# Optimization experiments

Measured on AMD Instinct MI355X. Metric: run time of the kernel, lower is better.

## Reference

```python
import jax, jax.numpy as jnp
import numpy as np

INPUT_DIM = 4096
BATCH = 64
E_PER = 262144  # edges per graph
MIN_SP = 0.3


def setup_inputs() -> dict:
    key = jax.random.key(0)
    k1, k2, k3 = jax.random.split(key, 3)
    E = BATCH * E_PER
    edge_index = jax.random.randint(k1, (2, E), 0, INPUT_DIM, dtype=jnp.int64)
    edge_attr = jax.random.normal(k2, (E,), dtype=jnp.float32)
    ptr = jnp.arange(BATCH + 1, dtype=jnp.int64)
    # learned parameter (xavier-normal-ish init)
    std = float(np.sqrt(2.0 / (INPUT_DIM + INPUT_DIM)))
    weight_mask = jax.random.normal(k3, (INPUT_DIM, INPUT_DIM), dtype=jnp.float32) * std
    return {"edge_index": edge_index, "edge_attr": edge_attr, "ptr": ptr, "weight_mask": weight_mask}


def reference(edge_index, edge_attr, ptr, weight_mask):
    B = ptr.shape[0] - 1
    E = edge_index.shape[1]
    e_per = E // B
    # symmetric sigmoid mask (dropout is None -> identity)
    sym = jax.nn.sigmoid(weight_mask.T + weight_mask)
    # x_reshape: [B, e_per]
    x = edge_attr.reshape(B, e_per)
    # edge_ind_reshape: [B, 2, e_per]
    ei = edge_index.T.reshape(B, e_per, 2).transpose(0, 2, 1)
    # gather mask weights for batch-0 edges
    src = ei[0, 0]
    dst = ei[0, 1]
    w = sym[src, dst]  # [e_per]
    num_rm = int(e_per * MIN_SP)  # static count of pruned edges
    order = jnp.argsort(w)
    pruned = order[:num_rm]
    kept = jnp.sort(order[num_rm:])  # boolean-mask compaction preserves order
    mask = jnp.ones((e_per,), dtype=bool).at[pruned].set(False)
    # filtered edge_index: [B, 2, K] -> permute(1,0,2) -> [2, B*K]
    fei = jnp.take(ei, kept, axis=2)
    out_edge_index = fei.transpose(1, 0, 2).reshape(2, -1)
    # filtered edge_attr: [B, K] -> [B*K]
    out_edge_attr = jnp.take(x, kept, axis=1).reshape(-1)
    return out_edge_index, out_edge_attr, mask
```

## Files before the change

kernel.cpp:

```cpp
#include <hip/hip_runtime.h>
#include <stdint.h>
#include <math.h>

#define CAND_CAP 8192
typedef unsigned long long ull;
typedef long long ll;
typedef unsigned int uint;
typedef float __attribute__((ext_vector_type(4))) f4;
typedef int __attribute__((ext_vector_type(4))) i4;

struct Ctrl {
  int sel0;
  int r0;
  int binsel;
  int r_in;
  int ncand;
  int pad;
  ull Tpack;
};

__device__ __forceinline__ uint fkey(float f) {
  uint u = __float_as_uint(f);
  return (u & 0x80000000u) ? ~u : (u | 0x80000000u);
}

__global__ void __launch_bounds__(256) k_keys(
    const int* __restrict__ ei, const float* __restrict__ wm,
    ll E, int D, uint* __restrict__ key32, uint* __restrict__ hist0) {
  __shared__ uint sh[256];
  int t = threadIdx.x;
  sh[t] = 0u;
  __syncthreads();
  int v = blockIdx.x * 256 + t;
  int4 s4 = ((const int4*)ei)[v];
  int4 d4 = ((const int4*)(ei + E))[v];
  float a0 = wm[(ll)s4.x * D + d4.x], b0 = wm[(ll)d4.x * D + s4.x];
  float a1 = wm[(ll)s4.y * D + d4.y], b1 = wm[(ll)d4.y * D + s4.y];
  float a2 = wm[(ll)s4.z * D + d4.z], b2 = wm[(ll)d4.z * D + s4.z];
  float a3 = wm[(ll)s4.w * D + d4.w], b3 = wm[(ll)d4.w * D + s4.w];
  uint4 k;
  k.x = fkey((float)((double)a0 + (double)b0));
  k.y = fkey((float)((double)a1 + (double)b1));
  k.z = fkey((float)((double)a2 + (double)b2));
  k.w = fkey((float)((double)a3 + (double)b3));
  ((uint4*)key32)[v] = k;
  atomicAdd(&sh[k.x >> 24], 1u);
  atomicAdd(&sh[k.y >> 24], 1u);
  atomicAdd(&sh[k.z >> 24], 1u);
  atomicAdd(&sh[k.w >> 24], 1u);
  __syncthreads();
  if (sh[t]) atomicAdd(&hist0[t], sh[t]);
}

__global__ void k_pick0(const uint* __restrict__ hist0, int r, Ctrl* ctrl) {
  __shared__ uint sh[256];
  int t = threadIdx.x;
  uint c = hist0[t];
  sh[t] = c;
  __syncthreads();
  for (int off = 1; off < 256; off <<= 1) {
    uint v = sh[t];
    uint a = (t >= off) ? sh[t - off] : 0u;
    __syncthreads();
    sh[t] = v + a;
    __syncthreads();
  }
  uint incl = sh[t], excl = incl - c;
  if ((uint)r >= excl && (uint)r < incl) {
    ctrl->sel0 = t;
    ctrl->r0 = (int)((uint)r - excl);
  }
}

__global__ void __launch_bounds__(256) k_hist1(
    const uint* __restrict__ key32, const Ctrl* __restrict__ ctrl,
    uint* __restrict__ hist1) {
  __shared__ uint sh[256];
  int t = threadIdx.x;
  sh[t] = 0u;
  __syncthreads();
  uint sel0 = (uint)ctrl->sel0;
  uint4 k = ((const uint4*)key32)[blockIdx.x * 256 + t];
  if ((k.x >> 24) == sel0) atomicAdd(&sh[(k.x >> 16) & 0xFFu], 1u);
  if ((k.y >> 24) == sel0) atomicAdd(&sh[(k.y >> 16) & 0xFFu], 1u);
  if ((k.z >> 24) == sel0) atomicAdd(&sh[(k.z >> 16) & 0xFFu], 1u);
  if ((k.w >> 24) == sel0) atomicAdd(&sh[(k.w >> 16) & 0xFFu], 1u);
  __syncthreads();
  if (sh[t]) atomicAdd(&hist1[t], sh[t]);
}

__global__ void k_pick1(const uint* __restrict__ hist1, Ctrl* ctrl) {
  __shared__ uint sh[256];
  int t = threadIdx.x;
  uint c = hist1[t];
  sh[t] = c;
  __syncthreads();
  for (int off = 1; off < 256; off <<= 1) {
    uint v = sh[t];
    uint a = (t >= off) ? sh[t - off] : 0u;
    __syncthreads();
    sh[t] = v + a;
    __syncthreads();
  }
  uint incl = sh[t], excl = incl - c;
  uint r = (uint)ctrl->r0;
  if (r >= excl && r < incl) {
    ctrl->binsel = (ctrl->sel0 << 8) | t;
    ctrl->r_in = (int)(r - excl);
  }
}

__global__ void k_cand(const uint* __restrict__ key32, int N, Ctrl* ctrl,
                       ull* __restrict__ cand) {
  int e = blockIdx.x * blockDim.x + threadIdx.x;
  if (e >= N) return;
  uint k = key32[e];
  if ((int)(k >> 16) == ctrl->binsel) {
    int p = atomicAdd(&ctrl->ncand, 1);
    if (p < CAND_CAP) cand[p] = ((ull)k << 32) | (uint)e;
  }
}

__global__ void k_pickT(const ull* __restrict__ cand, Ctrl* ctrl) {
  int nc = ctrl->ncand;
  if (nc > CAND_CAP) nc = CAND_CAP;
  int r = ctrl->r_in;
  for (int o = threadIdx.x; o < nc; o += blockDim.x) {
    ull my = cand[o];
    int cnt = 0;
    for (int i = 0; i < nc; ++i) cnt += (cand[i] < my) ? 1 : 0;
    if (cnt == r) ctrl->Tpack = my;
  }
}

__device__ __forceinline__ int keptf(uint k, int e, ull T) {
  return ((((ull)k << 32) | (uint)e) > T) ? 1 : 0;
}

__global__ void __launch_bounds__(256) k_scanA(
    const uint* __restrict__ key32, const Ctrl* __restrict__ ctrl,
    int* __restrict__ pw, int* __restrict__ bs, float* __restrict__ mask_out) {
  __shared__ int sh[256];
  int t = threadIdx.x, blk = blockIdx.x;
  ull T = ctrl->Tpack;
  uint4 k4 = ((const uint4*)key32)[blk * 256 + t];
  int e0 = blk * 1024 + t * 4;
  int f0 = keptf(k4.x, e0, T), f1 = keptf(k4.y, e0 + 1, T);
  int f2 = keptf(k4.z, e0 + 2, T), f3 = keptf(k4.w, e0 + 3, T);
  int c = f0 + f1 + f2 + f3;
  sh[t] = c;
  __syncthreads();
  for (int off = 1; off < 256; off <<= 1) {
    int v = sh[t];
    int a = (t >= off) ? sh[t - off] : 0;
    __syncthreads();
    sh[t] = v + a;
    __syncthreads();
  }
  int excl = sh[t] - c;
  pw[blk * 256 + t] = (excl << 4) | f0 | (f1 << 1) | (f2 << 2) | (f3 << 3);
  ((float4*)mask_out)[blk * 256 + t] =
      make_float4((float)f0, (float)f1, (float)f2, (float)f3);
  if (t == 255) bs[blk] = sh[255];
}

__global__ void k_scanB(int* bs, int nb) {
  __shared__ int sh[256];
  int t = threadIdx.x;
  int v = (t < nb) ? bs[t] : 0;
  sh[t] = v;
  __syncthreads();
  for (int off = 1; off < 256; off <<= 1) {
    int x = sh[t];
    int a = (t >= off) ? sh[t - off] : 0;
    __syncthreads();
    sh[t] = x + a;
    __syncthreads();
  }
  if (t < nb) bs[t] = sh[t] - v;
}

__global__ void __launch_bounds__(256) k_compact(
    const int* __restrict__ pw, const int* __restrict__ bs,
    const int* __restrict__ ei, const float* __restrict__ attr,
    ll E, int N, int Kkeep, ll BK, float* __restrict__ out) {
  __shared__ float lds[4][3][264];
  int t = threadIdx.x;
  int w = t >> 6;
  int l = t & 63;
  int blk = blockIdx.x, b = blockIdx.y;
  int q = blk * 256 + t;
  int wv = pw[q];
  int flags = wv & 15;
  int excl = wv >> 4;
  int subbase = __shfl(excl, 0);
  int wlast = __shfl(wv, 63);
  int cnt = (wlast >> 4) + __popc(wlast & 15) - subbase;
  ll cb = (ll)b * N;
  i4 d0 = __builtin_nontemporal_load((const i4*)(ei + cb) + q);
  i4 d1 = __builtin_nontemporal_load((const i4*)(ei + E + cb) + q);
  f4 d2 = __builtin_nontemporal_load((const f4*)(attr + cb) + q);
  ll ob = (ll)b * Kkeep + bs[blk] + subbase;
  int al = (int)(ob & 3);
  int p = (excl - subbase) + al;
  float* L0 = lds[w][0];
  float* L1 = lds[w][1];
  float* L2 = lds[w][2];
  if (flags & 1) { L0[p] = (float)d0.x; L1[p] = (float)d1.x; L2[p] = d2.x; p++; }
  if (flags & 2) { L0[p] = (float)d0.y; L1[p] = (float)d1.y; L2[p] = d2.y; p++; }
  if (flags & 4) { L0[p] = (float)d0.z; L1[p] = (float)d1.z; L2[p] = d2.z; p++; }
  if (flags & 8) { L0[p] = (float)d0.w; L1[p] = (float)d1.w; L2[p] = d2.w; }
  __threadfence_block();
  int lo = al, hi = al + cnt;
  int nslot = (hi + 3) >> 2;
  ll gbase = ob - al;
  #pragma unroll
  for (int r = 0; r < 3; ++r) {
    const float* src = lds[w][r];
    float* dst = out + (ll)r * BK + gbase;
    for (int i = l; i < nslot; i += 64) {
      int j0 = 4 * i;
      f4 v = *(const f4*)(src + j0);
      if (j0 >= lo && j0 + 3 < hi) {
        __builtin_nontemporal_store(v, (f4*)(dst + j0));
      } else {
        if (j0 >= lo && j0 < hi)         __builtin_nontemporal_store(v.x, dst + j0);
        if (j0 + 1 >= lo && j0 + 1 < hi) __builtin_nontemporal_store(v.y, dst + j0 + 1);
        if (j0 + 2 >= lo && j0 + 2 < hi) __builtin_nontemporal_store(v.z, dst + j0 + 2);
        if (j0 + 3 >= lo && j0 + 3 < hi) __builtin_nontemporal_store(v.w, dst + j0 + 3);
      }
    }
  }
}

extern "C" void kernel_launch(void* const* d_in, const int* in_sizes, int n_in,
                              void* d_out, int out_size, void* d_ws, size_t ws_size,
                              hipStream_t stream) {
  const int* ei = (const int*)d_in[0];
  const float* attr = (const float*)d_in[1];
  const float* wm = (const float*)d_in[3];

  int B = in_sizes[2] - 1;
  ll E = (ll)in_sizes[0] / 2;
  int e_per = (int)(E / B);
  int D = (int)llround(sqrt((double)in_sizes[3]));
  int num_rm = (int)((double)e_per * 0.3);
  int Kkeep = e_per - num_rm;
  ll BK = (ll)B * Kkeep;
  int nb = (e_per + 1023) / 1024;

  char* w = (char*)d_ws;
  size_t off = 0;
  uint* key32 = (uint*)(w + off);  off += (size_t)e_per * 4;
  uint* hist0 = (uint*)(w + off);  off += 256 * 4;
  uint* hist1 = (uint*)(w + off);  off += 256 * 4;
  Ctrl* ctrl = (Ctrl*)(w + off);   off += 64;
  ull* cand = (ull*)(w + off);     off += (size_t)CAND_CAP * 8;
  int* bs = (int*)(w + off);       off += 1024;
  int* pw = (int*)(w + off);       off += (size_t)(e_per / 4) * 4;
  (void)ws_size; (void)n_in; (void)out_size;

  float* out = (float*)d_out;
  float* mask_out = out + 3 * BK;

  hipMemsetAsync(hist0, 0, 256 * 4 + 256 * 4 + 64, stream);
  k_keys<<<dim3(e_per / 1024), dim3(256), 0, stream>>>(ei, wm, E, D, key32, hist0);
  k_pick0<<<dim3(1), dim3(256), 0, stream>>>(hist0, num_rm - 1, ctrl);
  k_hist1<<<dim3(e_per / 1024), dim3(256), 0, stream>>>(key32, ctrl, hist1);
  k_pick1<<<dim3(1), dim3(256), 0, stream>>>(hist1, ctrl);
  k_cand<<<dim3(nb), dim3(1024), 0, stream>>>(key32, e_per, ctrl, cand);
  k_pickT<<<dim3(1), dim3(1024), 0, stream>>>(cand, ctrl);
  k_scanA<<<dim3(nb), dim3(256), 0, stream>>>(key32, ctrl, pw, bs, mask_out);
  k_scanB<<<dim3(1), dim3(256), 0, stream>>>(bs, nb);
  k_compact<<<dim3(nb, B), dim3(256), 0, stream>>>(pw, bs, ei, attr,
                                                   E, e_per, Kkeep, BK, out);
}
```

Before: 117.7 us.

## Process several graphs per compact block with software-prefetched inputs

k_compact now loops over 8 batch graphs per block instead of one. The per-position flags, prefix offsets and block base are loaded once and reused across those graphs, and the next graph's edge and attribute vectors are prefetched while the current one is written out. Input loads switch from nontemporal to regular loads. The grid gets smaller and each thread holds more registers, and the per-wave LDS staging buffer is reused across iterations with no explicit fence.

```diff
diff --git a/kernel.cpp b/kernel.cpp
--- a/kernel.cpp
+++ b/kernel.cpp
@@ -183,12 +183,13 @@
 __global__ void __launch_bounds__(256) k_compact(
     const int* __restrict__ pw, const int* __restrict__ bs,
     const int* __restrict__ ei, const float* __restrict__ attr,
-    ll E, int N, int Kkeep, ll BK, float* __restrict__ out) {
+    ll E, int N, int Kkeep, ll BK, int BPG, float* __restrict__ out) {
   __shared__ float lds[4][3][264];
   int t = threadIdx.x;
   int w = t >> 6;
   int l = t & 63;
-  int blk = blockIdx.x, b = blockIdx.y;
+  int blk = blockIdx.x;
+  int b0 = blockIdx.y * BPG;
   int q = blk * 256 + t;
   int wv = pw[q];
   int flags = wv & 15;
@@ -196,40 +197,54 @@
   int subbase = __shfl(excl, 0);
   int wlast = __shfl(wv, 63);
   int cnt = (wlast >> 4) + __popc(wlast & 15) - subbase;
-  ll cb = (ll)b * N;
-  i4 d0 = __builtin_nontemporal_load((const i4*)(ei + cb) + q);
-  i4 d1 = __builtin_nontemporal_load((const i4*)(ei + E + cb) + q);
-  f4 d2 = __builtin_nontemporal_load((const f4*)(attr + cb) + q);
-  ll ob = (ll)b * Kkeep + bs[blk] + subbase;
-  int al = (int)(ob & 3);
-  int p = (excl - subbase) + al;
+  int poff = excl - subbase;
+  ll obase = (ll)bs[blk] + subbase;
   float* L0 = lds[w][0];
   float* L1 = lds[w][1];
   float* L2 = lds[w][2];
-  if (flags & 1) { L0[p] = (float)d0.x; L1[p] = (float)d1.x; L2[p] = d2.x; p++; }
-  if (flags & 2) { L0[p] = (float)d0.y; L1[p] = (float)d1.y; L2[p] = d2.y; p++; }
-  if (flags & 4) { L0[p] = (float)d0.z; L1[p] = (float)d1.z; L2[p] = d2.z; p++; }
-  if (flags & 8) { L0[p] = (float)d0.w; L1[p] = (float)d1.w; L2[p] = d2.w; }
-  __threadfence_block();
-  int lo = al, hi = al + cnt;
-  int nslot = (hi + 3) >> 2;
-  ll gbase = ob - al;
-  #pragma unroll
-  for (int r = 0; r < 3; ++r) {
-    const float* src = lds[w][r];
-    float* dst = out + (ll)r * BK + gbase;
-    for (int i = l; i < nslot; i += 64) {
-      int j0 = 4 * i;
-      f4 v = *(const f4*)(src + j0);
-      if (j0 >= lo && j0 + 3 < hi) {
-        __builtin_nontemporal_store(v, (f4*)(dst + j0));
-      } else {
-        if (j0 >= lo && j0 < hi)         __builtin_nontemporal_store(v.x, dst + j0);
-        if (j0 + 1 >= lo && j0 + 1 < hi) __builtin_nontemporal_store(v.y, dst + j0 + 1);
-        if (j0 + 2 >= lo && j0 + 2 < hi) __builtin_nontemporal_store(v.z, dst + j0 + 2);
-        if (j0 + 3 >= lo && j0 + 3 < hi) __builtin_nontemporal_store(v.w, dst + j0 + 3);
+
+  ll cb = (ll)b0 * N;
+  i4 d0 = *((const i4*)(ei + cb) + q);
+  i4 d1 = *((const i4*)(ei + E + cb) + q);
+  f4 d2 = *((const f4*)(attr + cb) + q);
+
+  for (int bi = 0; bi < BPG; ++bi) {
+    int b = b0 + bi;
+    ll ob = (ll)b * Kkeep + obase;
+    int al = (int)(ob & 3);
+    int p = poff + al;
+    if (flags & 1) { L0[p] = (float)d0.x; L1[p] = (float)d1.x; L2[p] = d2.x; p++; }
+    if (flags & 2) { L0[p] = (float)d0.y; L1[p] = (float)d1.y; L2[p] = d2.y; p++; }
+    if (flags & 4) { L0[p] = (float)d0.z; L1[p] = (float)d1.z; L2[p] = d2.z; p++; }
+    if (flags & 8) { L0[p] = (float)d0.w; L1[p] = (float)d1.w; L2[p] = d2.w; }
+    i4 n0, n1; f4 n2;
+    if (bi + 1 < BPG) {
+      ll cb2 = (ll)(b + 1) * N;
+      n0 = *((const i4*)(ei + cb2) + q);
+      n1 = *((const i4*)(ei + E + cb2) + q);
+      n2 = *((const f4*)(attr + cb2) + q);
+    }
+    int lo = al, hi = al + cnt;
+    int nslot = (hi + 3) >> 2;
+    ll gbase = ob - al;
+    #pragma unroll
+    for (int r = 0; r < 3; ++r) {
+      const float* src = lds[w][r];
+      float* dst = out + (ll)r * BK + gbase;
+      for (int i = l; i < nslot; i += 64) {
+        int j0 = 4 * i;
+        f4 v = *(const f4*)(src + j0);
+        if (j0 >= lo && j0 + 3 < hi) {
+          __builtin_nontemporal_store(v, (f4*)(dst + j0));
+        } else {
+          if (j0 >= lo && j0 < hi)         __builtin_nontemporal_store(v.x, dst + j0);
+          if (j0 + 1 >= lo && j0 + 1 < hi) __builtin_nontemporal_store(v.y, dst + j0 + 1);
+          if (j0 + 2 >= lo && j0 + 2 < hi) __builtin_nontemporal_store(v.z, dst + j0 + 2);
+          if (j0 + 3 >= lo && j0 + 3 < hi) __builtin_nontemporal_store(v.w, dst + j0 + 3);
+        }
       }
     }
+    d0 = n0; d1 = n1; d2 = n2;
   }
 }
 
@@ -263,6 +278,7 @@
   float* out = (float*)d_out;
   float* mask_out = out + 3 * BK;
 
+  int BPG = 8;
   hipMemsetAsync(hist0, 0, 256 * 4 + 256 * 4 + 64, stream);
   k_keys<<<dim3(e_per / 1024), dim3(256), 0, stream>>>(ei, wm, E, D, key32, hist0);
   k_pick0<<<dim3(1), dim3(256), 0, stream>>>(hist0, num_rm - 1, ctrl);
@@ -272,6 +288,6 @@
   k_pickT<<<dim3(1), dim3(1024), 0, stream>>>(cand, ctrl);
   k_scanA<<<dim3(nb), dim3(256), 0, stream>>>(key32, ctrl, pw, bs, mask_out);
   k_scanB<<<dim3(1), dim3(256), 0, stream>>>(bs, nb);
-  k_compact<<<dim3(nb, B), dim3(256), 0, stream>>>(pw, bs, ei, attr,
-                                                   E, e_per, Kkeep, BK, out);
-}
+  k_compact<<<dim3(nb, B / BPG), dim3(256), 0, stream>>>(pw, bs, ei, attr,
+                                                         E, e_per, Kkeep, BK, BPG, out);
+}
```

New measurement: 112.2 us, median of 3. 4.6% less time.
